# Kernel optimization log

Hardware: AMD Instinct MI355X
Metric: run time of the kernel (lower is better)

The kernel has to match this reference:

```python
import jax, jax.numpy as jnp
import numpy as np

NUM_USERS = 50000
NUM_ITEMS = 40000
EMB = 64
NNZ = 2_000_000
BATCH = 1024


def setup_inputs() -> dict:
    key = jax.random.key(0)
    ks = jax.random.split(key, 10)
    graph_rows = jax.random.randint(ks[0], (NNZ,), 0, NUM_USERS, dtype=jnp.int32)
    graph_cols = jax.random.randint(ks[1], (NNZ,), 0, NUM_ITEMS, dtype=jnp.int32)
    graph_vals = jax.random.uniform(ks[2], (NNZ,), dtype=jnp.float32)
    Wq = jax.random.normal(ks[3], (2 * EMB, NUM_ITEMS), dtype=jnp.float32) * 0.01
    bq = jnp.zeros((2 * EMB,), jnp.float32)
    Wp = jax.random.normal(ks[4], (NUM_ITEMS, EMB), dtype=jnp.float32) * 0.01
    bp = jnp.zeros((NUM_ITEMS,), jnp.float32)
    user = jax.random.randint(ks[5], (BATCH,), 0, NUM_USERS, dtype=jnp.int32)
    x = (jax.random.uniform(ks[6], (BATCH, NUM_ITEMS)) < 0.02).astype(jnp.float32)
    eps = jax.random.normal(ks[7], (NUM_USERS, EMB), dtype=jnp.float32)
    return dict(graph_vals=graph_vals, Wq=Wq, bq=bq, Wp=Wp, bp=bp, x=x,
                eps=eps, graph_rows=graph_rows, graph_cols=graph_cols, user=user)


def reference(graph_vals, Wq, bq, Wp, bp, x, eps, graph_rows, graph_cols, user):
    # ---- encode: single SpMM  h = Graph @ Wq^T + bq   (dropout off / eval mode)
    # gather item rows of Wq^T per nonzero, scale, scatter-add into users
    gathered = graph_vals[:, None] * Wq.T[graph_cols]          # [nnz, 2E]
    h = jax.ops.segment_sum(gathered, graph_rows, num_segments=NUM_USERS) + bq  # [U, 2E]
    mu, logvar = h[:, :EMB], h[:, EMB:]                        # [U, E] each
    # ---- reparameterize: z = mu + eps * exp(0.5*logvar)
    z = mu + eps * jnp.exp(0.5 * logvar)
    # ---- decode batch users: single Linear(E -> I)
    zb = z[user]                                               # [B, E]
    recon = zb @ Wp.T + bp                                     # [B, I]
    # ---- Mult-VAE ELBO (anneal = 1.0)
    log_sm = jax.nn.log_softmax(recon, axis=-1)
    recon_loss = -jnp.mean(jnp.sum(log_sm * x, axis=-1))
    mu_b, lv_b = mu[user], logvar[user]
    kl_loss = -0.5 * jnp.mean(jnp.sum(1.0 + lv_b - mu_b * mu_b - jnp.exp(lv_b), axis=-1))
    return jnp.stack([recon_loss, kl_loss])  # [2]: (recon_loss, KL_loss)
```

## Files before the change

### kernel.cpp

```cpp
#include <hip/hip_runtime.h>
#include <cstdint>

#define NUM_USERS 50000
#define NUM_ITEMS 40000
#define EMB 64
#define NNZ_E 2000000
#define BATCH 1024
#define NCHB 125
#define SLOT_CAP 128
#define INF_I 0x7fffffff

typedef __attribute__((ext_vector_type(8))) short short8;
typedef __attribute__((ext_vector_type(4))) float float4v;

__device__ __forceinline__ unsigned short f2bf(float f) {
    union { float f; unsigned u; } x; x.f = f;
    unsigned r = x.u + 0x7fffu + ((x.u >> 16) & 1u);
    return (unsigned short)(r >> 16);
}
__device__ __forceinline__ float bf2f(unsigned short s) {
    return __uint_as_float(((unsigned)s) << 16);
}

__global__ __launch_bounds__(256) void k_init(int* __restrict__ map, int* __restrict__ cnt,
                                              float* __restrict__ scal, int2* __restrict__ compact) {
    int t = blockIdx.x * blockDim.x + threadIdx.x;
    if (t < NUM_USERS) map[t] = INF_I;
    if (t < BATCH) cnt[t] = 0;
    if (t < 4) scal[t] = 0.f;
    if (t < BATCH * SLOT_CAP) compact[t] = make_int2(0, 0);
}

__global__ void k_map(const int* __restrict__ user, int* __restrict__ map) {
    int i = blockIdx.x * blockDim.x + threadIdx.x;
    if (i < BATCH) atomicMin(&map[user[i]], i);
}

__global__ __launch_bounds__(256) void k_prep(const float* __restrict__ Wq,
                                              const float* __restrict__ Wp,
                                              const float* __restrict__ bp,
                                              unsigned short* __restrict__ WqT,
                                              unsigned short* __restrict__ WpBf,
                                              unsigned short* __restrict__ WpT,
                                              unsigned short* __restrict__ bpBf) {
    __shared__ float t2f[160 * 65];
    const int bid = blockIdx.x;
    const int tid = threadIdx.x;
    if (bid < 1250) {
        const int jb = bid * 32;
        for (int idx = tid; idx < 4096; idx += 256) {
            int d = idx >> 5, c = idx & 31;
            t2f[d * 33 + c] = Wq[(size_t)d * NUM_ITEMS + jb + c];
        }
        __syncthreads();
        for (int idx = tid; idx < 4096; idx += 256) {
            int j = idx >> 7, d = idx & 127;
            WqT[(size_t)(jb + j) * 128 + d] = f2bf(t2f[d * 33 + j]);
        }
    } else if (bid < 3750) {
        const int e0 = ((bid - 1250) * 256 + tid) * 4;
        float4 w = *(const float4*)&Wp[e0];
        ushort4 o;
        o.x = f2bf(w.x); o.y = f2bf(w.y); o.z = f2bf(w.z); o.w = f2bf(w.w);
        *(ushort4*)&WpBf[e0] = o;
    } else if (bid < 4000) {
        const int j0 = (bid - 3750) * 160;
        for (int idx = tid; idx < 10240; idx += 256) {
            int jl = idx >> 6, d = idx & 63;
            t2f[jl * 65 + d] = Wp[(size_t)(j0 + jl) * 64 + d];
        }
        __syncthreads();
        for (int idx = tid; idx < 10240; idx += 256) {
            int d = idx / 160, jl = idx - d * 160;
            WpT[(size_t)d * NUM_ITEMS + j0 + jl] = f2bf(t2f[jl * 65 + d]);
        }
    } else {
        const int e0 = ((bid - 4000) * 256 + tid) * 4;
        if (e0 < NUM_ITEMS) {
            float4 w = *(const float4*)&bp[e0];
            ushort4 o;
            o.x = f2bf(w.x); o.y = f2bf(w.y); o.z = f2bf(w.z); o.w = f2bf(w.w);
            *(ushort4*)&bpBf[e0] = o;
        }
    }
}

__global__ __launch_bounds__(256) void k_scatter(const int* __restrict__ rows,
                                                 const int* __restrict__ cols,
                                                 const float* __restrict__ vals,
                                                 const int* __restrict__ map,
                                                 int* __restrict__ cnt,
                                                 int2* __restrict__ compact) {
    const int e = blockIdx.x * 256 + threadIdx.x;
    if (e >= NNZ_E) return;
    int s = map[rows[e]];
    if (s == INF_I) return;
    int pos = atomicAdd(&cnt[s], 1);
    if (pos < SLOT_CAP) compact[s * SLOT_CAP + pos] = make_int2(cols[e], __float_as_int(vals[e]));
}

__global__ __launch_bounds__(256) void k_hz(const int* __restrict__ user,
                                            const int* __restrict__ map,
                                            const int* __restrict__ cnt,
                                            const int2* __restrict__ compact,
                                            const unsigned short* __restrict__ WqT,
                                            const float* __restrict__ bq,
                                            const float* __restrict__ eps,
                                            unsigned short* __restrict__ zbBf,
                                            float* __restrict__ zF32,
                                            float* __restrict__ scal) {
    __shared__ float sh[4][128];
    const int i = blockIdx.x;
    const int tid = threadIdx.x;
    const int w = tid >> 6, lane = tid & 63;
    const int u = user[i];
    const int s = map[u];
    const int n8 = (min(cnt[s], SLOT_CAP) + 7) & ~7;
    const int2* cp = compact + s * SLOT_CAP;
    float ax = 0.f, ay = 0.f;
    for (int e = w; e < n8; e += 8) {
        int2 c0 = cp[e], c1 = cp[e + 4];
        ushort2 w0 = *(const ushort2*)&WqT[(size_t)c0.x * 128 + lane * 2];
        ushort2 w1 = *(const ushort2*)&WqT[(size_t)c1.x * 128 + lane * 2];
        float v0 = __int_as_float(c0.y), v1 = __int_as_float(c1.y);
        ax = fmaf(v0, bf2f(w0.x), ax);
        ay = fmaf(v0, bf2f(w0.y), ay);
        ax = fmaf(v1, bf2f(w1.x), ax);
        ay = fmaf(v1, bf2f(w1.y), ay);
    }
    sh[w][lane * 2] = ax;
    sh[w][lane * 2 + 1] = ay;
    __syncthreads();
    float h = 0.f;
    if (tid < 128) h = sh[0][tid] + sh[1][tid] + sh[2][tid] + sh[3][tid] + bq[tid];
    __syncthreads();
    if (tid < 128) sh[0][tid] = h;
    __syncthreads();
    if (tid < 64) {
        float mu = sh[0][tid];
        float lv = sh[0][tid + 64];
        float z = fmaf(eps[(size_t)u * EMB + tid], __expf(0.5f * lv), mu);
        zbBf[i * EMB + tid] = f2bf(z);
        zF32[i * EMB + tid] = z;
        float kl = 1.0f + lv - mu * mu - __expf(lv);
        #pragma unroll
        for (int o = 32; o; o >>= 1) kl += __shfl_down(kl, o);
        if (tid == 0) atomicAdd(&scal[1], kl);
    }
}

__global__ __launch_bounds__(256) void k_x(const float* __restrict__ x,
                                           const unsigned short* __restrict__ WpT,
                                           const unsigned short* __restrict__ bpBf,
                                           const float* __restrict__ zF32,
                                           float4* __restrict__ aux4) {
    const int tid = threadIdx.x;
    const int wid = tid >> 6, lane = tid & 63;
    const int l15 = lane & 15, quad = lane >> 4;
    const int kc = blockIdx.x;
    const int ibase = blockIdx.y * 128 + wid * 32;

    float4v acc[2][4], accA[2];
    #pragma unroll
    for (int mt = 0; mt < 2; mt++) {
        accA[mt] = (float4v){0.f, 0.f, 0.f, 0.f};
        #pragma unroll
        for (int nt = 0; nt < 4; nt++) acc[mt][nt] = (float4v){0.f, 0.f, 0.f, 0.f};
    }

    #pragma unroll
    for (int st = 0; st < 10; st++) {
        const int kb = kc * 320 + st * 32;
        short8 af[2];
        #pragma unroll
        for (int mt = 0; mt < 2; mt++) {
            const float* px = x + (size_t)(ibase + mt * 16 + l15) * NUM_ITEMS + kb + quad * 8;
            float4 a0 = *(const float4*)px;
            float4 a1 = *(const float4*)(px + 4);
            short8 v;
            v[0] = (short)f2bf(a0.x); v[1] = (short)f2bf(a0.y);
            v[2] = (short)f2bf(a0.z); v[3] = (short)f2bf(a0.w);
            v[4] = (short)f2bf(a1.x); v[5] = (short)f2bf(a1.y);
            v[6] = (short)f2bf(a1.z); v[7] = (short)f2bf(a1.w);
            af[mt] = v;
        }
        short8 bfr[4];
        #pragma unroll
        for (int nt = 0; nt < 4; nt++)
            bfr[nt] = *(const short8*)&WpT[(size_t)(nt * 16 + l15) * NUM_ITEMS + kb + quad * 8];
        short8 ab;
        if (l15 == 0) {
            ab = *(const short8*)&bpBf[kb + quad * 8];
        } else if (l15 == 1) {
            short o = (short)0x3F80;
            ab = (short8){o, o, o, o, o, o, o, o};
        } else {
            ab = (short8){0, 0, 0, 0, 0, 0, 0, 0};
        }
        #pragma unroll
        for (int mt = 0; mt < 2; mt++) {
            #pragma unroll
            for (int nt = 0; nt < 4; nt++)
                acc[mt][nt] = __builtin_amdgcn_mfma_f32_16x16x32_bf16(
                    af[mt], bfr[nt], acc[mt][nt], 0, 0, 0);
            accA[mt] = __builtin_amdgcn_mfma_f32_16x16x32_bf16(
                    af[mt], ab, accA[mt], 0, 0, 0);
        }
    }
    #pragma unroll
    for (int mt = 0; mt < 2; mt++) {
        #pragma unroll
        for (int r = 0; r < 4; r++) {
            const int row = ibase + mt * 16 + quad * 4 + r;
            float dxp = 0.f;
            #pragma unroll
            for (int nt = 0; nt < 4; nt++)
                dxp += zF32[(size_t)row * EMB + nt * 16 + l15] * acc[mt][nt][r];
            #pragma unroll
            for (int d = 1; d < 16; d <<= 1) dxp += __shfl_xor(dxp, d);
            float sxv = __shfl(accA[mt][r], (lane & 48) + 1);
            if (l15 == 0)
                aux4[(size_t)kc * BATCH + row] = make_float4(dxp, sxv, accA[mt][r], 0.f);
        }
    }
}

__global__ __launch_bounds__(256) void k_gemm(const unsigned short* __restrict__ zbBf,
                                              const unsigned short* __restrict__ WpBf,
                                              const float* __restrict__ bp,
                                              float2* __restrict__ part) {
    const int tid = threadIdx.x;
    const int wid = tid >> 6, lane = tid & 63;
    const int l15 = lane & 15, quad = lane >> 4;
    const int ibase = blockIdx.y * 128 + wid * 32;

    short8 af[2][2];
    #pragma unroll
    for (int mt = 0; mt < 2; mt++) {
        const unsigned short* pa = zbBf + (size_t)(ibase + mt * 16 + l15) * EMB + quad * 8;
        af[mt][0] = *(const short8*)pa;
        af[mt][1] = *(const short8*)(pa + 32);
    }

    float m_run[2][4], s_run[2][4];
    #pragma unroll
    for (int mt = 0; mt < 2; mt++)
        #pragma unroll
        for (int r = 0; r < 4; r++) { m_run[mt][r] = -1e30f; s_run[mt][r] = 0.f; }

    #pragma unroll
    for (int c5 = 0; c5 < 5; c5++) {
        const int jb = blockIdx.x * 320 + c5 * 64;
        short8 bfr[4][2];
        #pragma unroll
        for (int nt = 0; nt < 4; nt++) {
            const unsigned short* pb = WpBf + (size_t)(jb + nt * 16 + l15) * EMB + quad * 8;
            bfr[nt][0] = *(const short8*)pb;
            bfr[nt][1] = *(const short8*)(pb + 32);
        }
        float4v acc[2][4];
        #pragma unroll
        for (int mt = 0; mt < 2; mt++)
            #pragma unroll
            for (int nt = 0; nt < 4; nt++)
                acc[mt][nt] = (float4v){0.f, 0.f, 0.f, 0.f};
        #pragma unroll
        for (int kh = 0; kh < 2; kh++)
            #pragma unroll
            for (int mt = 0; mt < 2; mt++)
                #pragma unroll
                for (int nt = 0; nt < 4; nt++)
                    acc[mt][nt] = __builtin_amdgcn_mfma_f32_16x16x32_bf16(
                        af[mt][kh], bfr[nt][kh], acc[mt][nt], 0, 0, 0);
        float bpv[4];
        #pragma unroll
        for (int nt = 0; nt < 4; nt++) bpv[nt] = bp[jb + nt * 16 + l15];
        #pragma unroll
        for (int mt = 0; mt < 2; mt++) {
            #pragma unroll
            for (int r = 0; r < 4; r++) {
                float v0 = acc[mt][0][r] + bpv[0];
                float v1 = acc[mt][1][r] + bpv[1];
                float v2 = acc[mt][2][r] + bpv[2];
                float v3 = acc[mt][3][r] + bpv[3];
                float mx = fmaxf(fmaxf(v0, v1), fmaxf(v2, v3));
                float M2 = fmaxf(m_run[mt][r], mx);
                float ls = __expf(v0 - M2) + __expf(v1 - M2) +
                           __expf(v2 - M2) + __expf(v3 - M2);
                s_run[mt][r] = s_run[mt][r] * __expf(m_run[mt][r] - M2) + ls;
                m_run[mt][r] = M2;
            }
        }
    }
    #pragma unroll
    for (int d = 1; d < 16; d <<= 1) {
        #pragma unroll
        for (int mt = 0; mt < 2; mt++)
            #pragma unroll
            for (int r = 0; r < 4; r++) {
                float m2 = __shfl_xor(m_run[mt][r], d);
                float s2 = __shfl_xor(s_run[mt][r], d);
                float M = fmaxf(m_run[mt][r], m2);
                s_run[mt][r] = s_run[mt][r] * __expf(m_run[mt][r] - M)
                             + s2 * __expf(m2 - M);
                m_run[mt][r] = M;
            }
    }
    if (l15 == 0) {
        #pragma unroll
        for (int mt = 0; mt < 2; mt++)
            #pragma unroll
            for (int r = 0; r < 4; r++) {
                const int gi = ibase + mt * 16 + quad * 4 + r;
                part[(size_t)gi * NCHB + blockIdx.x] =
                    make_float2(m_run[mt][r], s_run[mt][r]);
            }
    }
}

__global__ __launch_bounds__(64) void k_merge(const float2* __restrict__ part,
                                              const float4* __restrict__ aux4,
                                              float* __restrict__ scal) {
    const int row = blockIdx.x;
    const int lane = threadIdx.x;
    float M = -1e30f, S = 0.f, dx = 0.f, sx = 0.f, xb = 0.f;
    for (int c = lane; c < NCHB; c += 64) {
        float2 p = part[(size_t)row * NCHB + c];
        float M2 = fmaxf(M, p.x);
        S = S * __expf(M - M2) + p.y * __expf(p.x - M2);
        M = M2;
        float4 a = aux4[(size_t)c * BATCH + row];
        dx += a.x; sx += a.y; xb += a.z;
    }
    #pragma unroll
    for (int o = 1; o < 64; o <<= 1) {
        float M2 = __shfl_xor(M, o);
        float S2 = __shfl_xor(S, o);
        float Mn = fmaxf(M, M2);
        S = S * __expf(M - Mn) + S2 * __expf(M2 - Mn);
        M = Mn;
        dx += __shfl_xor(dx, o);
        sx += __shfl_xor(sx, o);
        xb += __shfl_xor(xb, o);
    }
    if (lane == 0) {
        float lse = M + logf(S);
        float loss = dx + xb - lse * sx;
        atomicAdd(&scal[0], loss);
    }
}

__global__ void k_final(const float* __restrict__ scal, float* __restrict__ out) {
    if (threadIdx.x == 0 && blockIdx.x == 0) {
        out[0] = -scal[0] * (1.0f / BATCH);
        out[1] = -0.5f * scal[1] * (1.0f / BATCH);
    }
}

extern "C" void kernel_launch(void* const* d_in, const int* in_sizes, int n_in,
                              void* d_out, int out_size, void* d_ws, size_t ws_size,
                              hipStream_t stream) {
    const float* graph_vals = (const float*)d_in[0];
    const float* Wq         = (const float*)d_in[1];
    const float* bq         = (const float*)d_in[2];
    const float* Wp         = (const float*)d_in[3];
    const float* bp         = (const float*)d_in[4];
    const float* x          = (const float*)d_in[5];
    const float* eps        = (const float*)d_in[6];
    const int*   graph_rows = (const int*)d_in[7];
    const int*   graph_cols = (const int*)d_in[8];
    const int*   user       = (const int*)d_in[9];
    float* out = (float*)d_out;

    char* ws = (char*)d_ws;
    int*            map     = (int*)(ws + 0);
    int*            cnt     = (int*)(ws + 200704);
    float*          scal    = (float*)(ws + 204800);
    int2*           compact = (int2*)(ws + 205056);
    unsigned short* zbBf    = (unsigned short*)(ws + 1253632);
    float*          zF32    = (float*)(ws + 1384704);
    float2*         part    = (float2*)(ws + 1646848);
    unsigned short* WpBf    = (unsigned short*)(ws + 2670848);
    unsigned short* WqT     = (unsigned short*)(ws + 7790848);
    unsigned short* WpT     = (unsigned short*)(ws + 18030848);
    unsigned short* bpBf    = (unsigned short*)(ws + 23150848);
    float4*         aux4    = (float4*)(ws + 23230848);

    k_init<<<512, 256, 0, stream>>>(map, cnt, scal, compact);
    k_map<<<4, 256, 0, stream>>>(user, map);
    k_prep<<<4040, 256, 0, stream>>>(Wq, Wp, bp, WqT, WpBf, WpT, bpBf);
    k_scatter<<<7813, 256, 0, stream>>>(graph_rows, graph_cols, graph_vals, map, cnt, compact);
    k_hz<<<BATCH, 256, 0, stream>>>(user, map, cnt, compact, WqT, bq, eps, zbBf, zF32, scal);
    dim3 g(NCHB, BATCH / 128);
    k_x<<<g, 256, 0, stream>>>(x, WpT, bpBf, zF32, aux4);
    k_gemm<<<g, 256, 0, stream>>>(zbBf, WpBf, bp, part);
    k_merge<<<BATCH, 64, 0, stream>>>(part, aux4, scal);
    k_final<<<1, 64, 0, stream>>>(scal, out);
}
```

Measured before the change: 385.0 us.

## Fuse scatter into prep, merge x-pass with logits GEMM, fold final into merge

```diff
diff --git a/kernel.cpp b/kernel.cpp
--- a/kernel.cpp
+++ b/kernel.cpp
@@ -9,6 +9,7 @@
 #define NCHB 125
 #define SLOT_CAP 128
 #define INF_I 0x7fffffff
+#define SC_BLK 7813
 
 typedef __attribute__((ext_vector_type(8))) short short8;
 typedef __attribute__((ext_vector_type(4))) float float4v;
@@ -20,6 +21,9 @@
 }
 __device__ __forceinline__ float bf2f(unsigned short s) {
     return __uint_as_float(((unsigned)s) << 16);
+}
+__device__ __forceinline__ unsigned pack01(float lo, float hi) {
+    return __builtin_amdgcn_perm(__float_as_uint(hi), __float_as_uint(lo), 0x07060302u);
 }
 
 __global__ __launch_bounds__(256) void k_init(int* __restrict__ map, int* __restrict__ cnt,
@@ -36,18 +40,34 @@
     if (i < BATCH) atomicMin(&map[user[i]], i);
 }
 
-__global__ __launch_bounds__(256) void k_prep(const float* __restrict__ Wq,
-                                              const float* __restrict__ Wp,
-                                              const float* __restrict__ bp,
-                                              unsigned short* __restrict__ WqT,
-                                              unsigned short* __restrict__ WpBf,
-                                              unsigned short* __restrict__ WpT,
-                                              unsigned short* __restrict__ bpBf) {
+__global__ __launch_bounds__(256) void k_prepsc(const int* __restrict__ rows,
+                                                const int* __restrict__ cols,
+                                                const float* __restrict__ vals,
+                                                const int* __restrict__ map,
+                                                int* __restrict__ cnt,
+                                                int2* __restrict__ compact,
+                                                const float* __restrict__ Wq,
+                                                const float* __restrict__ Wp,
+                                                const float* __restrict__ bp,
+                                                unsigned short* __restrict__ WqT,
+                                                unsigned short* __restrict__ WpBf,
+                                                unsigned short* __restrict__ WpT,
+                                                unsigned short* __restrict__ bpBf) {
     __shared__ float t2f[160 * 65];
     const int bid = blockIdx.x;
     const int tid = threadIdx.x;
-    if (bid < 1250) {
-        const int jb = bid * 32;
+    if (bid < SC_BLK) {
+        const int e = bid * 256 + tid;
+        if (e >= NNZ_E) return;
+        int s = map[rows[e]];
+        if (s == INF_I) return;
+        int pos = atomicAdd(&cnt[s], 1);
+        if (pos < SLOT_CAP) compact[s * SLOT_CAP + pos] = make_int2(cols[e], __float_as_int(vals[e]));
+        return;
+    }
+    const int pb = bid - SC_BLK;
+    if (pb < 1250) {
+        const int jb = pb * 32;
         for (int idx = tid; idx < 4096; idx += 256) {
             int d = idx >> 5, c = idx & 31;
             t2f[d * 33 + c] = Wq[(size_t)d * NUM_ITEMS + jb + c];
@@ -57,14 +77,14 @@
             int j = idx >> 7, d = idx & 127;
             WqT[(size_t)(jb + j) * 128 + d] = f2bf(t2f[d * 33 + j]);
         }
-    } else if (bid < 3750) {
-        const int e0 = ((bid - 1250) * 256 + tid) * 4;
+    } else if (pb < 3750) {
+        const int e0 = ((pb - 1250) * 256 + tid) * 4;
         float4 w = *(const float4*)&Wp[e0];
         ushort4 o;
         o.x = f2bf(w.x); o.y = f2bf(w.y); o.z = f2bf(w.z); o.w = f2bf(w.w);
         *(ushort4*)&WpBf[e0] = o;
-    } else if (bid < 4000) {
-        const int j0 = (bid - 3750) * 160;
+    } else if (pb < 4000) {
+        const int j0 = (pb - 3750) * 160;
         for (int idx = tid; idx < 10240; idx += 256) {
             int jl = idx >> 6, d = idx & 63;
             t2f[jl * 65 + d] = Wp[(size_t)(j0 + jl) * 64 + d];
@@ -75,7 +95,7 @@
             WpT[(size_t)d * NUM_ITEMS + j0 + jl] = f2bf(t2f[jl * 65 + d]);
         }
     } else {
-        const int e0 = ((bid - 4000) * 256 + tid) * 4;
+        const int e0 = ((pb - 4000) * 256 + tid) * 4;
         if (e0 < NUM_ITEMS) {
             float4 w = *(const float4*)&bp[e0];
             ushort4 o;
@@ -83,20 +103,6 @@
             *(ushort4*)&bpBf[e0] = o;
         }
     }
-}
-
-__global__ __launch_bounds__(256) void k_scatter(const int* __restrict__ rows,
-                                                 const int* __restrict__ cols,
-                                                 const float* __restrict__ vals,
-                                                 const int* __restrict__ map,
-                                                 int* __restrict__ cnt,
-                                                 int2* __restrict__ compact) {
-    const int e = blockIdx.x * 256 + threadIdx.x;
-    if (e >= NNZ_E) return;
-    int s = map[rows[e]];
-    if (s == INF_I) return;
-    int pos = atomicAdd(&cnt[s], 1);
-    if (pos < SLOT_CAP) compact[s * SLOT_CAP + pos] = make_int2(cols[e], __float_as_int(vals[e]));
 }
 
 __global__ __launch_bounds__(256) void k_hz(const int* __restrict__ user,
@@ -149,11 +155,14 @@
     }
 }
 
-__global__ __launch_bounds__(256) void k_x(const float* __restrict__ x,
-                                           const unsigned short* __restrict__ WpT,
-                                           const unsigned short* __restrict__ bpBf,
-                                           const float* __restrict__ zF32,
-                                           float4* __restrict__ aux4) {
+__global__ __launch_bounds__(256) void k_xz(const float* __restrict__ x,
+                                            const unsigned short* __restrict__ WpT,
+                                            const unsigned short* __restrict__ bpBf,
+                                            const float* __restrict__ zF32,
+                                            const unsigned short* __restrict__ zbBf,
+                                            const unsigned short* __restrict__ WpBf,
+                                            const float* __restrict__ bp,
+                                            float4* __restrict__ part4) {
     const int tid = threadIdx.x;
     const int wid = tid >> 6, lane = tid & 63;
     const int l15 = lane & 15, quad = lane >> 4;
@@ -167,7 +176,6 @@
         #pragma unroll
         for (int nt = 0; nt < 4; nt++) acc[mt][nt] = (float4v){0.f, 0.f, 0.f, 0.f};
     }
-
     #pragma unroll
     for (int st = 0; st < 10; st++) {
         const int kb = kc * 320 + st * 32;
@@ -177,12 +185,12 @@
             const float* px = x + (size_t)(ibase + mt * 16 + l15) * NUM_ITEMS + kb + quad * 8;
             float4 a0 = *(const float4*)px;
             float4 a1 = *(const float4*)(px + 4);
-            short8 v;
-            v[0] = (short)f2bf(a0.x); v[1] = (short)f2bf(a0.y);
-            v[2] = (short)f2bf(a0.z); v[3] = (short)f2bf(a0.w);
-            v[4] = (short)f2bf(a1.x); v[5] = (short)f2bf(a1.y);
-            v[6] = (short)f2bf(a1.z); v[7] = (short)f2bf(a1.w);
-            af[mt] = v;
+            union { short8 s; unsigned u[4]; } v;
+            v.u[0] = pack01(a0.x, a0.y);
+            v.u[1] = pack01(a0.z, a0.w);
+            v.u[2] = pack01(a1.x, a1.y);
+            v.u[3] = pack01(a1.z, a1.w);
+            af[mt] = v.s;
         }
         short8 bfr[4];
         #pragma unroll
@@ -207,6 +215,7 @@
                     af[mt], ab, accA[mt], 0, 0, 0);
         }
     }
+    float c_s[2][4], sx_s[2][4];
     #pragma unroll
     for (int mt = 0; mt < 2; mt++) {
         #pragma unroll
@@ -218,30 +227,18 @@
                 dxp += zF32[(size_t)row * EMB + nt * 16 + l15] * acc[mt][nt][r];
             #pragma unroll
             for (int d = 1; d < 16; d <<= 1) dxp += __shfl_xor(dxp, d);
-            float sxv = __shfl(accA[mt][r], (lane & 48) + 1);
-            if (l15 == 0)
-                aux4[(size_t)kc * BATCH + row] = make_float4(dxp, sxv, accA[mt][r], 0.f);
-        }
-    }
-}
-
-__global__ __launch_bounds__(256) void k_gemm(const unsigned short* __restrict__ zbBf,
-                                              const unsigned short* __restrict__ WpBf,
-                                              const float* __restrict__ bp,
-                                              float2* __restrict__ part) {
-    const int tid = threadIdx.x;
-    const int wid = tid >> 6, lane = tid & 63;
-    const int l15 = lane & 15, quad = lane >> 4;
-    const int ibase = blockIdx.y * 128 + wid * 32;
-
-    short8 af[2][2];
+            sx_s[mt][r] = __shfl(accA[mt][r], (lane & 48) + 1);
+            c_s[mt][r] = dxp + accA[mt][r];
+        }
+    }
+
+    short8 zf[2][2];
     #pragma unroll
     for (int mt = 0; mt < 2; mt++) {
         const unsigned short* pa = zbBf + (size_t)(ibase + mt * 16 + l15) * EMB + quad * 8;
-        af[mt][0] = *(const short8*)pa;
-        af[mt][1] = *(const short8*)(pa + 32);
-    }
-
+        zf[mt][0] = *(const short8*)pa;
+        zf[mt][1] = *(const short8*)(pa + 32);
+    }
     float m_run[2][4], s_run[2][4];
     #pragma unroll
     for (int mt = 0; mt < 2; mt++)
@@ -250,28 +247,28 @@
 
     #pragma unroll
     for (int c5 = 0; c5 < 5; c5++) {
-        const int jb = blockIdx.x * 320 + c5 * 64;
-        short8 bfr[4][2];
+        const int jb = kc * 320 + c5 * 64;
+        short8 bfr2[4][2];
         #pragma unroll
         for (int nt = 0; nt < 4; nt++) {
             const unsigned short* pb = WpBf + (size_t)(jb + nt * 16 + l15) * EMB + quad * 8;
-            bfr[nt][0] = *(const short8*)pb;
-            bfr[nt][1] = *(const short8*)(pb + 32);
-        }
-        float4v acc[2][4];
+            bfr2[nt][0] = *(const short8*)pb;
+            bfr2[nt][1] = *(const short8*)(pb + 32);
+        }
+        float4v accz[2][4];
         #pragma unroll
         for (int mt = 0; mt < 2; mt++)
             #pragma unroll
             for (int nt = 0; nt < 4; nt++)
-                acc[mt][nt] = (float4v){0.f, 0.f, 0.f, 0.f};
+                accz[mt][nt] = (float4v){0.f, 0.f, 0.f, 0.f};
         #pragma unroll
         for (int kh = 0; kh < 2; kh++)
             #pragma unroll
             for (int mt = 0; mt < 2; mt++)
                 #pragma unroll
                 for (int nt = 0; nt < 4; nt++)
-                    acc[mt][nt] = __builtin_amdgcn_mfma_f32_16x16x32_bf16(
-                        af[mt][kh], bfr[nt][kh], acc[mt][nt], 0, 0, 0);
+                    accz[mt][nt] = __builtin_amdgcn_mfma_f32_16x16x32_bf16(
+                        zf[mt][kh], bfr2[nt][kh], accz[mt][nt], 0, 0, 0);
         float bpv[4];
         #pragma unroll
         for (int nt = 0; nt < 4; nt++) bpv[nt] = bp[jb + nt * 16 + l15];
@@ -279,10 +276,10 @@
         for (int mt = 0; mt < 2; mt++) {
             #pragma unroll
             for (int r = 0; r < 4; r++) {
-                float v0 = acc[mt][0][r] + bpv[0];
-                float v1 = acc[mt][1][r] + bpv[1];
-                float v2 = acc[mt][2][r] + bpv[2];
-                float v3 = acc[mt][3][r] + bpv[3];
+                float v0 = accz[mt][0][r] + bpv[0];
+                float v1 = accz[mt][1][r] + bpv[1];
+                float v2 = accz[mt][2][r] + bpv[2];
+                float v3 = accz[mt][3][r] + bpv[3];
                 float mx = fmaxf(fmaxf(v0, v1), fmaxf(v2, v3));
                 float M2 = fmaxf(m_run[mt][r], mx);
                 float ls = __expf(v0 - M2) + __expf(v1 - M2) +
@@ -311,26 +308,24 @@
         for (int mt = 0; mt < 2; mt++)
             #pragma unroll
             for (int r = 0; r < 4; r++) {
-                const int gi = ibase + mt * 16 + quad * 4 + r;
-                part[(size_t)gi * NCHB + blockIdx.x] =
-                    make_float2(m_run[mt][r], s_run[mt][r]);
+                const int row = ibase + mt * 16 + quad * 4 + r;
+                part4[(size_t)row * NCHB + kc] =
+                    make_float4(m_run[mt][r], s_run[mt][r], c_s[mt][r], sx_s[mt][r]);
             }
     }
 }
 
-__global__ __launch_bounds__(64) void k_merge(const float2* __restrict__ part,
-                                              const float4* __restrict__ aux4,
-                                              float* __restrict__ scal) {
+__global__ __launch_bounds__(64) void k_merge(const float4* __restrict__ part4,
+                                              float* __restrict__ scal,
+                                              float* __restrict__ out) {
     const int row = blockIdx.x;
     const int lane = threadIdx.x;
-    float M = -1e30f, S = 0.f, dx = 0.f, sx = 0.f, xb = 0.f;
+    float M = -1e30f, S = 0.f, dxc = 0.f, sx = 0.f;
     for (int c = lane; c < NCHB; c += 64) {
-        float2 p = part[(size_t)row * NCHB + c];
+        float4 p = part4[(size_t)row * NCHB + c];
         float M2 = fmaxf(M, p.x);
         S = S * __expf(M - M2) + p.y * __expf(p.x - M2);
-        M = M2;
-        float4 a = aux4[(size_t)c * BATCH + row];
-        dx += a.x; sx += a.y; xb += a.z;
+        M = M2; dxc += p.z; sx += p.w;
     }
     #pragma unroll
     for (int o = 1; o < 64; o <<= 1) {
@@ -339,21 +334,20 @@
         float Mn = fmaxf(M, M2);
         S = S * __expf(M - Mn) + S2 * __expf(M2 - Mn);
         M = Mn;
-        dx += __shfl_xor(dx, o);
+        dxc += __shfl_xor(dxc, o);
         sx += __shfl_xor(sx, o);
-        xb += __shfl_xor(xb, o);
     }
     if (lane == 0) {
         float lse = M + logf(S);
-        float loss = dx + xb - lse * sx;
-        atomicAdd(&scal[0], loss);
-    }
-}
-
-__global__ void k_final(const float* __restrict__ scal, float* __restrict__ out) {
-    if (threadIdx.x == 0 && blockIdx.x == 0) {
-        out[0] = -scal[0] * (1.0f / BATCH);
-        out[1] = -0.5f * scal[1] * (1.0f / BATCH);
+        atomicAdd(&scal[0], dxc - lse * sx);
+        __threadfence();
+        unsigned done = atomicAdd((unsigned*)&scal[2], 1u);
+        if (done == BATCH - 1) {
+            float recon = atomicAdd(&scal[0], 0.f);
+            float kl = atomicAdd(&scal[1], 0.f);
+            out[0] = -recon * (1.0f / BATCH);
+            out[1] = -0.5f * kl * (1.0f / BATCH);
+        }
     }
 }
 
@@ -379,21 +373,18 @@
     int2*           compact = (int2*)(ws + 205056);
     unsigned short* zbBf    = (unsigned short*)(ws + 1253632);
     float*          zF32    = (float*)(ws + 1384704);
-    float2*         part    = (float2*)(ws + 1646848);
-    unsigned short* WpBf    = (unsigned short*)(ws + 2670848);
-    unsigned short* WqT     = (unsigned short*)(ws + 7790848);
-    unsigned short* WpT     = (unsigned short*)(ws + 18030848);
-    unsigned short* bpBf    = (unsigned short*)(ws + 23150848);
-    float4*         aux4    = (float4*)(ws + 23230848);
+    float4*         part4   = (float4*)(ws + 1646848);
+    unsigned short* WpBf    = (unsigned short*)(ws + 3694848);
+    unsigned short* WqT     = (unsigned short*)(ws + 8814848);
+    unsigned short* WpT     = (unsigned short*)(ws + 19054848);
+    unsigned short* bpBf    = (unsigned short*)(ws + 24174848);
 
     k_init<<<512, 256, 0, stream>>>(map, cnt, scal, compact);
     k_map<<<4, 256, 0, stream>>>(user, map);
-    k_prep<<<4040, 256, 0, stream>>>(Wq, Wp, bp, WqT, WpBf, WpT, bpBf);
-    k_scatter<<<7813, 256, 0, stream>>>(graph_rows, graph_cols, graph_vals, map, cnt, compact);
+    k_prepsc<<<SC_BLK + 4040, 256, 0, stream>>>(graph_rows, graph_cols, graph_vals, map, cnt,
+                                                compact, Wq, Wp, bp, WqT, WpBf, WpT, bpBf);
     k_hz<<<BATCH, 256, 0, stream>>>(user, map, cnt, compact, WqT, bq, eps, zbBf, zF32, scal);
     dim3 g(NCHB, BATCH / 128);
-    k_x<<<g, 256, 0, stream>>>(x, WpT, bpBf, zF32, aux4);
-    k_gemm<<<g, 256, 0, stream>>>(zbBf, WpBf, bp, part);
-    k_merge<<<BATCH, 64, 0, stream>>>(part, aux4, scal);
-    k_final<<<1, 64, 0, stream>>>(scal, out);
-}
+    k_xz<<<g, 256, 0, stream>>>(x, WpT, bpBf, zF32, zbBf, WpBf, bp, part4);
+    k_merge<<<BATCH, 64, 0, stream>>>(part4, scal, out);
+}
```

Result: no change. 388.9 us (+1.0%).
